# Optimization experiments

Hardware: AMD Instinct MI355X
Metric: run time of the kernel (lower is better)

The kernel has to match this reference:

```python
import jax, jax.numpy as jnp
import numpy as np

B, IN_DIM, Q_DIM, CODE_DIM, K, PROJ_DIM = 8192, 512, 128, 1024, 8, 64
NUM_LAYERS = 5
THRESHOLD = 0.9
SPARSITY_LEVELS = list(map(int, np.linspace(5, CODE_DIM, K)))  # matches torch default


def setup_inputs() -> dict:
    key = jax.random.key(0)
    ks = jax.random.split(key, 9)
    s = 0.02
    return {
        "x": jax.random.normal(ks[0], (B, IN_DIM), jnp.float32),
        "Wq": jax.random.normal(ks[1], (IN_DIM, Q_DIM), jnp.float32) * s,
        "bq": jnp.zeros((Q_DIM,), jnp.float32),
        "keys": jax.random.normal(ks[2], (K, Q_DIM), jnp.float32) * s,
        "We": jax.random.normal(ks[3], (K, IN_DIM, CODE_DIM), jnp.float32) * s,
        "S": jax.random.normal(ks[4], (K, CODE_DIM, CODE_DIM), jnp.float32) * s,
        "theta": jax.random.uniform(ks[5], (K,), jnp.float32) * 0.01,
        "W1": jax.random.normal(ks[6], (CODE_DIM, CODE_DIM), jnp.float32) * s,
        "b1": jnp.zeros((CODE_DIM,), jnp.float32),
        "W2": jax.random.normal(ks[7], (CODE_DIM, PROJ_DIM), jnp.float32) * s,
        "b2": jnp.zeros((PROJ_DIM,), jnp.float32),
    }


def _soft(z, theta):
    return jnp.sign(z) * jnp.maximum(jnp.abs(z) - theta, 0.0)


def reference(x, Wq, bq, keys, We, S, theta, W1, b1, W2, b2):
    # --- gating (attention): softmax(q @ keys^T / sqrt(d)) -> (B, K)
    q = x @ Wq + bq
    scores = (q @ keys.T) / jnp.sqrt(jnp.asarray(Q_DIM, x.dtype))
    gating_probs = jax.nn.softmax(scores, axis=-1)

    # --- all K LISTA experts densely: zs has shape (K, B, code_dim)
    Bx = jnp.einsum('bi,kic->kbc', x, We)            # (K, B, C)
    th = theta[:, None, None]
    z = _soft(Bx, th)
    for _ in range(NUM_LAYERS):
        z = _soft(Bx + jnp.einsum('kbc,kcd->kbd', z, S), th)

    # hard top-k (sparsity_level) magnitude pruning per expert
    pruned = []
    for k in range(K):
        zk = z[k]
        kk = SPARSITY_LEVELS[k]
        az = jnp.abs(zk)
        kth = jax.lax.top_k(az, kk)[0][:, -1]         # (B,)
        pruned.append(jnp.where(az >= kth[:, None], zk, 0.0))
    zs = jnp.stack(pruned, axis=0)                    # (K, B, C)

    # --- hard gating: among experts with p >= threshold*p_max, pick the
    # one with the smallest sparsity level (argmax always eligible, so the
    # empty-eligible branch in the torch code is unreachable for threshold<=1)
    p_max = jnp.max(gating_probs, axis=-1, keepdims=True)
    eligible = gating_probs >= THRESHOLD * p_max      # (B, K)
    sl = jnp.asarray(SPARSITY_LEVELS, jnp.float32)
    idx = jnp.argmin(jnp.where(eligible, sl[None, :], jnp.inf), axis=-1)  # (B,)

    selected_z = jnp.take_along_axis(zs, idx[None, :, None], axis=0)[0]   # (B, C)

    # --- projection head
    h = jax.nn.relu(selected_z @ W1 + b1)
    return h @ W2 + b2
```

## Files before the change

### kernel.cpp

```cpp
#include <hip/hip_runtime.h>
#include <math.h>

#define NB 8192
#define IND 512
#define QDIM 128
#define CD 1024
#define KE 8
#define PD 64
#define ORB 32

typedef _Float16 h8 __attribute__((ext_vector_type(8)));
typedef _Float16 h4 __attribute__((ext_vector_type(4)));
typedef float fx16 __attribute__((ext_vector_type(16)));

#define GLD16(g, l) __builtin_amdgcn_global_load_lds((const __attribute__((address_space(1))) void*)(g), (__attribute__((address_space(3))) void*)(l), 16, 0, 0)

__device__ __forceinline__ float softt(float v, float th) {
    float a = fabsf(v) - th;
    return a > 0.0f ? copysignf(a, v) : 0.0f;
}

__device__ __forceinline__ void fsplit(float v, _Float16& hi, _Float16& lo) {
    hi = (_Float16)v;
    lo = (_Float16)((v - (float)hi) * 2048.0f);
}

__global__ void k_precompute_M(const float* __restrict__ Wq, const float* __restrict__ keys,
                               const float* __restrict__ bq, float* __restrict__ M,
                               float* __restrict__ sb) {
    const float RSQ = 0.088388347648318447f;
    int g = blockIdx.x * 256 + threadIdx.x;
    if (g < IND * KE) {
        int i = g >> 3, k = g & 7;
        float s = 0.f;
        for (int q = 0; q < QDIM; ++q) s += Wq[i * QDIM + q] * keys[k * QDIM + q];
        M[g] = s * RSQ;
    }
    if (blockIdx.x == 0 && threadIdx.x < KE) {
        int k = threadIdx.x;
        float s = 0.f;
        for (int q = 0; q < QDIM; ++q) s += bq[q] * keys[k * QDIM + q];
        sb[k] = s * RSQ;
    }
}

__global__ __launch_bounds__(256)
void k_scores(const float* __restrict__ x, const float* __restrict__ M,
              const float* __restrict__ sb, int* __restrict__ idx) {
    __shared__ float Ms[KE][IND];
    __shared__ float sbs[KE];
    int t = threadIdx.x;
    #pragma unroll
    for (int j = 0; j < 16; ++j) {
        int e = j * 256 + t;
        Ms[e & 7][e >> 3] = M[e];
    }
    if (t < KE) sbs[t] = sb[t];
    __syncthreads();
    int w = t >> 6, lane = t & 63;
    int row = blockIdx.x * 4 + w;
    const float* xr = x + (size_t)row * IND;
    float sc[KE];
    #pragma unroll
    for (int k = 0; k < KE; ++k) sc[k] = 0.f;
    #pragma unroll
    for (int j = 0; j < IND / 64; ++j) {
        int ii = lane + 64 * j;
        float xv = xr[ii];
        #pragma unroll
        for (int k = 0; k < KE; ++k) sc[k] += xv * Ms[k][ii];
    }
    #pragma unroll
    for (int k = 0; k < KE; ++k) {
        #pragma unroll
        for (int off = 32; off >= 1; off >>= 1) sc[k] += __shfl_down(sc[k], off, 64);
    }
    if (lane == 0) {
        float smax = -1e30f;
        #pragma unroll
        for (int k = 0; k < KE; ++k) { sc[k] += sbs[k]; smax = fmaxf(smax, sc[k]); }
        const float LN09 = -0.105360515657826301f;
        int e = 0;
        #pragma unroll
        for (int k = KE - 1; k >= 0; --k)
            if (sc[k] >= smax + LN09) e = k;
        idx[row] = e;
    }
}

__global__ __launch_bounds__(256)
void k_count(const int* __restrict__ idx, int* __restrict__ perm,
             int* __restrict__ counts, int* __restrict__ offsets) {
    __shared__ int hist[256][KE];
    __shared__ int sc[2][KE][256];
    __shared__ int base[KE];
    const int t = threadIdx.x;
    int pc[KE];
    #pragma unroll
    for (int e = 0; e < KE; ++e) pc[e] = 0;
    for (int j = 0; j < NB / 256; ++j) pc[idx[j * 256 + t]]++;
    #pragma unroll
    for (int e = 0; e < KE; ++e) { hist[t][e] = pc[e]; sc[0][e][t] = pc[e]; }
    __syncthreads();
    int cur = 0;
    for (int d = 1; d < 256; d <<= 1) {
        #pragma unroll
        for (int e = 0; e < KE; ++e) {
            int v = sc[cur][e][t];
            if (t >= d) v += sc[cur][e][t - d];
            sc[cur ^ 1][e][t] = v;
        }
        cur ^= 1;
        __syncthreads();
    }
    if (t == 0) {
        int a = 0;
        #pragma unroll
        for (int e = 0; e < KE; ++e) {
            int tot = sc[cur][e][255];
            base[e] = a; offsets[e] = a; counts[e] = tot; a += tot;
        }
    }
    __syncthreads();
    int pos[KE];
    #pragma unroll
    for (int e = 0; e < KE; ++e) pos[e] = base[e] + sc[cur][e][t] - hist[t][e];
    for (int j = 0; j < NB / 256; ++j) {
        int r = j * 256 + t;
        int e = idx[r];
        perm[pos[e]++] = r;
    }
}

__global__ __launch_bounds__(256)
void k_split_rows(const float* __restrict__ src, _Float16* __restrict__ ph,
                  _Float16* __restrict__ pl, int n) {
    int i = (blockIdx.x * 256 + threadIdx.x) * 4;
    if (i < n) {
        float4 v = *(const float4*)(src + i);
        h4 hh, ll;
        #pragma unroll
        for (int j = 0; j < 4; ++j) {
            _Float16 a, b;
            fsplit((&v.x)[j], a, b);
            hh[j] = a; ll[j] = b;
        }
        *(h4*)(ph + i) = hh;
        *(h4*)(pl + i) = ll;
    }
}

__global__ __launch_bounds__(256)
void k_tsplit(const float* __restrict__ src, _Float16* __restrict__ th,
              _Float16* __restrict__ tl, int K, const int* __restrict__ counts) {
    int e = blockIdx.z;
    if (counts[e] == 0) return;
    __shared__ float tile[64][65];
    int k0 = blockIdx.x * 64;
    int n0 = blockIdx.y * 64;
    const float* s = src + (size_t)e * K * CD;
    int t = threadIdx.x;
    int tr = t >> 4;
    int tc = (t & 15) * 4;
    #pragma unroll
    for (int p = 0; p < 4; ++p) {
        int kk = tr + p * 16;
        float4 v = *(const float4*)&s[(size_t)(k0 + kk) * CD + n0 + tc];
        #pragma unroll
        for (int j = 0; j < 4; ++j) tile[kk][tc + j] = (&v.x)[j];
    }
    __syncthreads();
    int n = t >> 2;
    int kq = (t & 3) * 16;
    h8 hh0, hh1, ll0, ll1;
    #pragma unroll
    for (int j = 0; j < 8; ++j) {
        _Float16 a, b;
        fsplit(tile[kq + j][n], a, b);
        hh0[j] = a; ll0[j] = b;
        fsplit(tile[kq + 8 + j][n], a, b);
        hh1[j] = a; ll1[j] = b;
    }
    size_t ob = ((size_t)e * CD + n0 + n) * K + k0 + kq;
    *(h8*)(th + ob) = hh0;
    *(h8*)(th + ob + 8) = hh1;
    *(h8*)(tl + ob) = ll0;
    *(h8*)(tl + ob + 8) = ll1;
}

template <int KDIM, int MODE>
__global__ __launch_bounds__(256)
void k_mfma(const _Float16* __restrict__ Ah, const _Float16* __restrict__ Al,
            const _Float16* __restrict__ Bh, const _Float16* __restrict__ Bl,
            const float* __restrict__ theta, const float* __restrict__ BxBuf,
            float* __restrict__ BxOut, _Float16* __restrict__ zh, _Float16* __restrict__ zl,
            float* __restrict__ zf,
            const int* __restrict__ perm, const int* __restrict__ counts,
            const int* __restrict__ offsets) {
    const int e = blockIdx.z;
    const int cnt = counts[e];
    const int p = blockIdx.x + 8 * blockIdx.y;
    const int gx = p & 7;
    const int qq = p >> 3;
    const int bxl = qq & 7;
    const int byl = gx + 8 * (qq >> 3);
    const int m0 = byl * 128;
    if (m0 >= cnt) return;
    const int n0 = bxl * 128;
    const int off = offsets[e];
    const float th = theta[e];

    __shared__ _Float16 Asl[2][128 * 64];
    __shared__ _Float16 Bsl[2][128 * 64];

    const int t = threadIdx.x;
    const int lane = t & 63;
    const int w = t >> 6;

    const _Float16* aptr[4];
    const _Float16* bptr[4];
    #pragma unroll
    for (int i = 0; i < 4; ++i) {
        int s = w * 4 + i;
        int r = s * 8 + (lane >> 3);
        int pc = lane & 7;
        int lc = pc ^ ((r ^ (r >> 3)) & 7);
        int comp = lc & 1;
        int kg = lc >> 1;
        int mrow = m0 + r; if (mrow > cnt - 1) mrow = cnt - 1;
        size_t grow;
        if constexpr (MODE == 0) grow = (size_t)perm[off + mrow];
        else grow = (size_t)(off + mrow);
        aptr[i] = (comp ? Al : Ah) + grow * KDIM + kg * 8;
        bptr[i] = (comp ? Bl : Bh) + ((size_t)e * CD + n0 + r) * KDIM + kg * 8;
    }

    const int wm = w >> 1, wn = w & 1;
    const int q = lane >> 5;
    const int ml = lane & 31;

    fx16 acc1[2][2], acc2[2][2];
    #pragma unroll
    for (int mt = 0; mt < 2; ++mt)
        #pragma unroll
        for (int nt = 0; nt < 2; ++nt)
            #pragma unroll
            for (int g = 0; g < 16; ++g) { acc1[mt][nt][g] = 0.f; acc2[mt][nt][g] = 0.f; }

    auto stage = [&](int kt, int buf) {
        const int koff = kt * 32;
        #pragma unroll
        for (int i = 0; i < 4; ++i) {
            GLD16(aptr[i] + koff, &Asl[buf][(w * 4 + i) * 512]);
            GLD16(bptr[i] + koff, &Bsl[buf][(w * 4 + i) * 512]);
        }
    };

    const int NT = KDIM / 32;
    stage(0, 0);
    __syncthreads();
    for (int kt = 0; kt < NT; ++kt) {
        const int buf = kt & 1;
        if (kt + 1 < NT) stage(kt + 1, buf ^ 1);
        #pragma unroll
        for (int ks = 0; ks < 2; ++ks) {
            const int base = ks * 4 + q * 2;
            h8 ah[2], al2[2], bh2[2], bl2[2];
            #pragma unroll
            for (int mt = 0; mt < 2; ++mt) {
                int row = wm * 64 + mt * 32 + ml;
                int sw = (row ^ (row >> 3)) & 7;
                int mb = row * 64;
                ah[mt]  = *(const h8*)&Asl[buf][mb + (((base + 0) ^ sw) * 8)];
                al2[mt] = *(const h8*)&Asl[buf][mb + (((base + 1) ^ sw) * 8)];
            }
            #pragma unroll
            for (int nt = 0; nt < 2; ++nt) {
                int col = wn * 64 + nt * 32 + ml;
                int sw = (col ^ (col >> 3)) & 7;
                int nb = col * 64;
                bh2[nt] = *(const h8*)&Bsl[buf][nb + (((base + 0) ^ sw) * 8)];
                bl2[nt] = *(const h8*)&Bsl[buf][nb + (((base + 1) ^ sw) * 8)];
            }
            #pragma unroll
            for (int mt = 0; mt < 2; ++mt)
                #pragma unroll
                for (int nt = 0; nt < 2; ++nt) {
                    acc1[mt][nt] = __builtin_amdgcn_mfma_f32_32x32x16_f16(ah[mt],  bh2[nt], acc1[mt][nt], 0, 0, 0);
                    acc2[mt][nt] = __builtin_amdgcn_mfma_f32_32x32x16_f16(ah[mt],  bl2[nt], acc2[mt][nt], 0, 0, 0);
                    acc2[mt][nt] = __builtin_amdgcn_mfma_f32_32x32x16_f16(al2[mt], bh2[nt], acc2[mt][nt], 0, 0, 0);
                }
        }
        __syncthreads();
    }

    const float LSC = 4.8828125e-4f;
    #pragma unroll
    for (int mt = 0; mt < 2; ++mt)
        #pragma unroll
        for (int nt = 0; nt < 2; ++nt) {
            #pragma unroll
            for (int g = 0; g < 16; ++g) {
                int rl = wm * 64 + mt * 32 + (g & 3) + 8 * (g >> 2) + 4 * q;
                int mrow = m0 + rl;
                if (mrow < cnt) {
                    int col = n0 + wn * 64 + nt * 32 + ml;
                    size_t addr = (size_t)(off + mrow) * CD + col;
                    float v = acc1[mt][nt][g] + acc2[mt][nt][g] * LSC;
                    if constexpr (MODE == 0) {
                        BxOut[addr] = v;
                        float z = softt(v, th);
                        _Float16 a, b;
                        fsplit(z, a, b);
                        zh[addr] = a; zl[addr] = b;
                    } else if constexpr (MODE == 1) {
                        float z = softt(v + BxBuf[addr], th);
                        _Float16 a, b;
                        fsplit(z, a, b);
                        zh[addr] = a; zl[addr] = b;
                    } else {
                        zf[addr] = softt(v + BxBuf[addr], th);
                    }
                }
            }
        }
}

__global__ __launch_bounds__(256)
void k_prune(const float* __restrict__ z, const int* __restrict__ offsets,
             float* __restrict__ cval, int* __restrict__ cidx, int* __restrict__ rcnt) {
    const int SL[KE] = {5, 150, 296, 441, 587, 732, 878, 1024};
    const int t = threadIdx.x;
    const int lane = t & 63;
    const int wv = t >> 6;
    const int slot = blockIdx.x * 4 + wv;
    int k = 0;
    #pragma unroll
    for (int e = 1; e < KE; ++e)
        if (slot >= offsets[e]) k = e;
    const int lvl = SL[k];
    const float* zr = z + (size_t)slot * CD;
    float v[16];
    unsigned ab[16];
    #pragma unroll
    for (int j = 0; j < 16; ++j) {
        v[j] = zr[lane + 64 * j];
        ab[j] = __float_as_uint(fabsf(v[j]));
    }
    unsigned thr = 0;
    for (int b = 30; b >= 0; --b) {
        unsigned cand = thr | (1u << b);
        int c = 0;
        #pragma unroll
        for (int j = 0; j < 16; ++j) c += (ab[j] >= cand) ? 1 : 0;
        #pragma unroll
        for (int off = 1; off < 64; off <<= 1) c += __shfl_xor(c, off, 64);
        if (c >= lvl) thr = cand;
    }
    float* cvr = cval + (size_t)slot * CD;
    int* cir = cidx + (size_t)slot * CD;
    int base = 0;
    #pragma unroll
    for (int j = 0; j < 16; ++j) {
        bool keep = ab[j] >= thr;
        unsigned long long m = __ballot(keep);
        if (keep) {
            int pos = base + __popcll(m & ((1ULL << lane) - 1));
            cvr[pos] = v[j];
            cir[pos] = lane + 64 * j;
        }
        base += __popcll(m);
    }
    if (lane == 0) rcnt[slot] = base;
}

__global__ __launch_bounds__(256)
void k_output(const float* __restrict__ cval, const int* __restrict__ cidx,
              const int* __restrict__ rcnt,
              const float* __restrict__ W1, const float* __restrict__ b1,
              const float* __restrict__ W2, const float* __restrict__ b2,
              const int* __restrict__ perm, float* __restrict__ out) {
    __shared__ float W2s[64][68];
    __shared__ float hTs[64][34];
    __shared__ float cvS[ORB][16];
    __shared__ int   ciS[ORB][16];
    __shared__ int   cnS[ORB];

    const int t = threadIdx.x;
    const int s0 = blockIdx.x * ORB;

    if (t < ORB) cnS[t] = rcnt[s0 + t];
    __syncthreads();
    #pragma unroll
    for (int u = t; u < ORB * 16; u += 256) {
        int r = u >> 4, e = u & 15;
        int cnt = cnS[r];
        cvS[r][e] = (e < cnt) ? cval[(size_t)(s0 + r) * CD + e] : 0.f;
        ciS[r][e] = (e < cnt) ? cidx[(size_t)(s0 + r) * CD + e] : 0;
    }

    const int tm = t >> 4;
    const int tn = t & 15;
    const int iL = t & 63;
    const int rs = t >> 6;

    float acc0[4], acc1[4];
    #pragma unroll
    for (int j = 0; j < 4; ++j) { acc0[j] = 0.f; acc1[j] = 0.f; }

    for (int ch = 0; ch < 16; ++ch) {
        const int i0 = ch * 64;
        __syncthreads();
        #pragma unroll
        for (int p = 0; p < 4; ++p) {
            int kr = (t >> 4) + 16 * p;
            float4 w = *(const float4*)&W2[(size_t)(i0 + kr) * PD + (t & 15) * 4];
            *(float4*)&W2s[kr][(t & 15) * 4] = w;
        }
        float bv = b1[i0 + iL];
        #pragma unroll
        for (int jj = 0; jj < 8; ++jj) {
            int r = rs * 8 + jj;
            int cnt = cnS[r];
            float acc = bv;
            float wv[16];
            #pragma unroll
            for (int e = 0; e < 16; ++e)
                wv[e] = W1[(size_t)ciS[r][e] * CD + i0 + iL];
            #pragma unroll
            for (int e = 0; e < 16; ++e)
                acc = fmaf(cvS[r][e], wv[e], acc);
            if (cnt > 16) {
                const float* cvr = cval + (size_t)(s0 + r) * CD;
                const int* cir = cidx + (size_t)(s0 + r) * CD;
                for (int e = 16; e < cnt; ++e)
                    acc = fmaf(cvr[e], W1[(size_t)cir[e] * CD + i0 + iL], acc);
            }
            hTs[iL][r] = fmaxf(acc, 0.f);
        }
        __syncthreads();
        #pragma unroll 8
        for (int i = 0; i < 64; ++i) {
            float2 h2 = *(const float2*)&hTs[i][2 * tm];
            float4 w4 = *(const float4*)&W2s[i][4 * tn];
            const float* wp = &w4.x;
            #pragma unroll
            for (int j = 0; j < 4; ++j) {
                acc0[j] = fmaf(h2.x, wp[j], acc0[j]);
                acc1[j] = fmaf(h2.y, wp[j], acc1[j]);
            }
        }
    }

    float4 bb = *(const float4*)&b2[4 * tn];
    const float* bp = &bb.x;
    int g0 = perm[s0 + 2 * tm];
    int g1 = perm[s0 + 2 * tm + 1];
    float4 o0, o1;
    #pragma unroll
    for (int j = 0; j < 4; ++j) { (&o0.x)[j] = acc0[j] + bp[j]; (&o1.x)[j] = acc1[j] + bp[j]; }
    *(float4*)&out[(size_t)g0 * PD + 4 * tn] = o0;
    *(float4*)&out[(size_t)g1 * PD + 4 * tn] = o1;
}

extern "C" void kernel_launch(void* const* d_in, const int* in_sizes, int n_in,
                              void* d_out, int out_size, void* d_ws, size_t ws_size,
                              hipStream_t stream) {
    const float* x     = (const float*)d_in[0];
    const float* Wq    = (const float*)d_in[1];
    const float* bq    = (const float*)d_in[2];
    const float* keys  = (const float*)d_in[3];
    const float* We    = (const float*)d_in[4];
    const float* S     = (const float*)d_in[5];
    const float* theta = (const float*)d_in[6];
    const float* W1    = (const float*)d_in[7];
    const float* b1    = (const float*)d_in[8];
    const float* W2    = (const float*)d_in[9];
    const float* b2    = (const float*)d_in[10];
    float* out = (float*)d_out;

    const size_t F = (size_t)NB * CD;
    float* Bx = (float*)d_ws;
    _Float16* zAh = (_Float16*)(Bx + F);
    _Float16* zAl = zAh + F;
    float* R1 = (float*)(zAl + F);
    _Float16* xh  = (_Float16*)R1;
    _Float16* xl  = xh + (size_t)NB * IND;
    _Float16* weh = xl + (size_t)NB * IND;
    _Float16* wel = weh + (size_t)KE * IND * CD;
    _Float16* zBh = (_Float16*)R1;
    _Float16* zBl = zBh + F;
    float* z1 = R1;
    _Float16* sth = (_Float16*)(R1 + F);
    _Float16* stl = sth + F;
    float* M  = (float*)(stl + F);
    float* sb = M + IND * KE;
    int* idx     = (int*)(sb + 8);
    int* perm    = idx + NB;
    int* counts  = perm + NB;
    int* offsets = counts + KE;
    int* rcnt    = offsets + KE;
    float* cval = Bx;
    int*   cidx = (int*)zAh;

    k_precompute_M<<<16, 256, 0, stream>>>(Wq, keys, bq, M, sb);
    k_scores<<<NB / 4, 256, 0, stream>>>(x, M, sb, idx);
    k_count<<<1, 256, 0, stream>>>(idx, perm, counts, offsets);

    k_split_rows<<<(NB * IND) / 1024, 256, 0, stream>>>(x, xh, xl, NB * IND);
    {
        dim3 g(IND / 64, CD / 64, KE);
        k_tsplit<<<g, 256, 0, stream>>>(We, weh, wel, IND, counts);
    }
    {
        dim3 g(CD / 64, CD / 64, KE);
        k_tsplit<<<g, 256, 0, stream>>>(S, sth, stl, CD, counts);
    }

    dim3 gg(CD / 128, NB / 128, KE);
    k_mfma<IND, 0><<<gg, 256, 0, stream>>>(xh, xl, weh, wel, theta, nullptr, Bx, zAh, zAl, nullptr, perm, counts, offsets);
    k_mfma<CD, 1><<<gg, 256, 0, stream>>>(zAh, zAl, sth, stl, theta, Bx, nullptr, zBh, zBl, nullptr, perm, counts, offsets);
    k_mfma<CD, 1><<<gg, 256, 0, stream>>>(zBh, zBl, sth, stl, theta, Bx, nullptr, zAh, zAl, nullptr, perm, counts, offsets);
    k_mfma<CD, 1><<<gg, 256, 0, stream>>>(zAh, zAl, sth, stl, theta, Bx, nullptr, zBh, zBl, nullptr, perm, counts, offsets);
    k_mfma<CD, 1><<<gg, 256, 0, stream>>>(zBh, zBl, sth, stl, theta, Bx, nullptr, zAh, zAl, nullptr, perm, counts, offsets);
    k_mfma<CD, 2><<<gg, 256, 0, stream>>>(zAh, zAl, sth, stl, theta, Bx, nullptr, nullptr, nullptr, z1, perm, counts, offsets);

    k_prune<<<NB / 4, 256, 0, stream>>>(z1, offsets, cval, cidx, rcnt);
    k_output<<<NB / ORB, 256, 0, stream>>>(cval, cidx, rcnt, W1, b1, W2, b2, perm, out);
}
```

Measured before the change: 677.3 us.

## Fuse top-k pruning with sparse projection head into one per-row kernel

Merges the prune and output kernels into a single kernel in which each wavefront handles one row. It computes the magnitude threshold with ballot popcounts, compacts the kept entries into LDS, and accumulates the W1 rows for those entries straight into registers. It then applies ReLU and does the W2 projection in the same wavefront. This drops the compacted value/index round trip through global memory and one launch. In exchange, each row streams W1 rows with no cross-row reuse, and rows with more than 160 nonzeros fall back to a dense 1024-row loop, which could be costly for experts with high sparsity levels.

```diff
diff --git a/kernel.cpp b/kernel.cpp
--- a/kernel.cpp
+++ b/kernel.cpp
@@ -7,7 +7,7 @@
 #define CD 1024
 #define KE 8
 #define PD 64
-#define ORB 32
+#define PCAP 160
 
 typedef _Float16 h8 __attribute__((ext_vector_type(8)));
 typedef _Float16 h4 __attribute__((ext_vector_type(4)));
@@ -327,18 +327,28 @@
 }
 
 __global__ __launch_bounds__(256)
-void k_prune(const float* __restrict__ z, const int* __restrict__ offsets,
-             float* __restrict__ cval, int* __restrict__ cidx, int* __restrict__ rcnt) {
+void k_po(const float* __restrict__ z, const int* __restrict__ offsets,
+          const float* __restrict__ W1, const float* __restrict__ b1,
+          const float* __restrict__ W2, const float* __restrict__ b2,
+          const int* __restrict__ perm, float* __restrict__ out) {
     const int SL[KE] = {5, 150, 296, 441, 587, 732, 878, 1024};
+    __shared__ float vLg[4][PCAP];
+    __shared__ int   iLg[4][PCAP];
+    __shared__ float hSg[4][CD];
     const int t = threadIdx.x;
     const int lane = t & 63;
     const int wv = t >> 6;
     const int slot = blockIdx.x * 4 + wv;
+    float* vL = vLg[wv];
+    int* iLs = iLg[wv];
+    float* hS = hSg[wv];
+
     int k = 0;
     #pragma unroll
     for (int e = 1; e < KE; ++e)
         if (slot >= offsets[e]) k = e;
     const int lvl = SL[k];
+
     const float* zr = z + (size_t)slot * CD;
     float v[16];
     unsigned ab[16];
@@ -352,115 +362,75 @@
         unsigned cand = thr | (1u << b);
         int c = 0;
         #pragma unroll
-        for (int j = 0; j < 16; ++j) c += (ab[j] >= cand) ? 1 : 0;
-        #pragma unroll
-        for (int off = 1; off < 64; off <<= 1) c += __shfl_xor(c, off, 64);
+        for (int j = 0; j < 16; ++j)
+            c += __popcll(__ballot(ab[j] >= cand));
         if (c >= lvl) thr = cand;
     }
-    float* cvr = cval + (size_t)slot * CD;
-    int* cir = cidx + (size_t)slot * CD;
-    int base = 0;
-    #pragma unroll
-    for (int j = 0; j < 16; ++j) {
-        bool keep = ab[j] >= thr;
-        unsigned long long m = __ballot(keep);
-        if (keep) {
-            int pos = base + __popcll(m & ((1ULL << lane) - 1));
-            cvr[pos] = v[j];
-            cir[pos] = lane + 64 * j;
-        }
-        base += __popcll(m);
-    }
-    if (lane == 0) rcnt[slot] = base;
-}
-
-__global__ __launch_bounds__(256)
-void k_output(const float* __restrict__ cval, const int* __restrict__ cidx,
-              const int* __restrict__ rcnt,
-              const float* __restrict__ W1, const float* __restrict__ b1,
-              const float* __restrict__ W2, const float* __restrict__ b2,
-              const int* __restrict__ perm, float* __restrict__ out) {
-    __shared__ float W2s[64][68];
-    __shared__ float hTs[64][34];
-    __shared__ float cvS[ORB][16];
-    __shared__ int   ciS[ORB][16];
-    __shared__ int   cnS[ORB];
-
-    const int t = threadIdx.x;
-    const int s0 = blockIdx.x * ORB;
-
-    if (t < ORB) cnS[t] = rcnt[s0 + t];
-    __syncthreads();
-    #pragma unroll
-    for (int u = t; u < ORB * 16; u += 256) {
-        int r = u >> 4, e = u & 15;
-        int cnt = cnS[r];
-        cvS[r][e] = (e < cnt) ? cval[(size_t)(s0 + r) * CD + e] : 0.f;
-        ciS[r][e] = (e < cnt) ? cidx[(size_t)(s0 + r) * CD + e] : 0;
-    }
-
-    const int tm = t >> 4;
-    const int tn = t & 15;
-    const int iL = t & 63;
-    const int rs = t >> 6;
-
-    float acc0[4], acc1[4];
-    #pragma unroll
-    for (int j = 0; j < 4; ++j) { acc0[j] = 0.f; acc1[j] = 0.f; }
-
-    for (int ch = 0; ch < 16; ++ch) {
-        const int i0 = ch * 64;
-        __syncthreads();
-        #pragma unroll
-        for (int p = 0; p < 4; ++p) {
-            int kr = (t >> 4) + 16 * p;
-            float4 w = *(const float4*)&W2[(size_t)(i0 + kr) * PD + (t & 15) * 4];
-            *(float4*)&W2s[kr][(t & 15) * 4] = w;
-        }
-        float bv = b1[i0 + iL];
-        #pragma unroll
-        for (int jj = 0; jj < 8; ++jj) {
-            int r = rs * 8 + jj;
-            int cnt = cnS[r];
-            float acc = bv;
-            float wv[16];
-            #pragma unroll
-            for (int e = 0; e < 16; ++e)
-                wv[e] = W1[(size_t)ciS[r][e] * CD + i0 + iL];
-            #pragma unroll
-            for (int e = 0; e < 16; ++e)
-                acc = fmaf(cvS[r][e], wv[e], acc);
-            if (cnt > 16) {
-                const float* cvr = cval + (size_t)(s0 + r) * CD;
-                const int* cir = cidx + (size_t)(s0 + r) * CD;
-                for (int e = 16; e < cnt; ++e)
-                    acc = fmaf(cvr[e], W1[(size_t)cir[e] * CD + i0 + iL], acc);
+    int cnt = 0;
+    #pragma unroll
+    for (int j = 0; j < 16; ++j) cnt += __popcll(__ballot(ab[j] >= thr));
+
+    float h[16];
+    #pragma unroll
+    for (int j = 0; j < 16; ++j) h[j] = b1[lane + 64 * j];
+
+    if (cnt <= PCAP) {
+        int base = 0;
+        #pragma unroll
+        for (int j = 0; j < 16; ++j) {
+            bool keep = ab[j] >= thr;
+            unsigned long long m = __ballot(keep);
+            if (keep) {
+                int pos = base + __popcll(m & ((1ULL << lane) - 1));
+                vL[pos] = v[j];
+                iLs[pos] = lane + 64 * j;
             }
-            hTs[iL][r] = fmaxf(acc, 0.f);
-        }
-        __syncthreads();
-        #pragma unroll 8
-        for (int i = 0; i < 64; ++i) {
-            float2 h2 = *(const float2*)&hTs[i][2 * tm];
-            float4 w4 = *(const float4*)&W2s[i][4 * tn];
-            const float* wp = &w4.x;
-            #pragma unroll
-            for (int j = 0; j < 4; ++j) {
-                acc0[j] = fmaf(h2.x, wp[j], acc0[j]);
-                acc1[j] = fmaf(h2.y, wp[j], acc1[j]);
-            }
-        }
-    }
-
-    float4 bb = *(const float4*)&b2[4 * tn];
-    const float* bp = &bb.x;
-    int g0 = perm[s0 + 2 * tm];
-    int g1 = perm[s0 + 2 * tm + 1];
-    float4 o0, o1;
-    #pragma unroll
-    for (int j = 0; j < 4; ++j) { (&o0.x)[j] = acc0[j] + bp[j]; (&o1.x)[j] = acc1[j] + bp[j]; }
-    *(float4*)&out[(size_t)g0 * PD + 4 * tn] = o0;
-    *(float4*)&out[(size_t)g1 * PD + 4 * tn] = o1;
+            base += __popcll(m);
+        }
+        __builtin_amdgcn_wave_barrier();
+        for (int e = 0; e < cnt; ++e) {
+            float val = vL[e];
+            const float* wr = W1 + (size_t)iLs[e] * CD;
+            #pragma unroll
+            for (int j = 0; j < 16; ++j)
+                h[j] = fmaf(val, wr[lane + 64 * j], h[j]);
+        }
+    } else {
+        #pragma unroll
+        for (int j = 0; j < 16; ++j)
+            hS[lane + 64 * j] = (ab[j] >= thr) ? v[j] : 0.f;
+        __builtin_amdgcn_wave_barrier();
+        for (int e = 0; e < CD; ++e) {
+            float val = hS[e];
+            const float* wr = W1 + (size_t)e * CD;
+            #pragma unroll
+            for (int j = 0; j < 16; ++j)
+                h[j] = fmaf(val, wr[lane + 64 * j], h[j]);
+        }
+        __builtin_amdgcn_wave_barrier();
+    }
+
+    #pragma unroll
+    for (int j = 0; j < 16; ++j) hS[lane + 64 * j] = fmaxf(h[j], 0.f);
+    __builtin_amdgcn_wave_barrier();
+
+    const float* w2c = W2 + lane;
+    float a0 = 0.f, a1 = 0.f, a2 = 0.f, a3 = 0.f, a4 = 0.f, a5 = 0.f, a6 = 0.f, a7 = 0.f;
+    #pragma unroll 4
+    for (int i = 0; i < CD; i += 8) {
+        float4 h0 = *(const float4*)&hS[i];
+        float4 h1 = *(const float4*)&hS[i + 4];
+        a0 = fmaf(h0.x, w2c[(size_t)(i + 0) * PD], a0);
+        a1 = fmaf(h0.y, w2c[(size_t)(i + 1) * PD], a1);
+        a2 = fmaf(h0.z, w2c[(size_t)(i + 2) * PD], a2);
+        a3 = fmaf(h0.w, w2c[(size_t)(i + 3) * PD], a3);
+        a4 = fmaf(h1.x, w2c[(size_t)(i + 4) * PD], a4);
+        a5 = fmaf(h1.y, w2c[(size_t)(i + 5) * PD], a5);
+        a6 = fmaf(h1.z, w2c[(size_t)(i + 6) * PD], a6);
+        a7 = fmaf(h1.w, w2c[(size_t)(i + 7) * PD], a7);
+    }
+    float acc = ((a0 + a1) + (a2 + a3)) + ((a4 + a5) + (a6 + a7)) + b2[lane];
+    out[(size_t)perm[slot] * PD + lane] = acc;
 }
 
 extern "C" void kernel_launch(void* const* d_in, const int* in_sizes, int n_in,
@@ -499,9 +469,6 @@
     int* perm    = idx + NB;
     int* counts  = perm + NB;
     int* offsets = counts + KE;
-    int* rcnt    = offsets + KE;
-    float* cval = Bx;
-    int*   cidx = (int*)zAh;
 
     k_precompute_M<<<16, 256, 0, stream>>>(Wq, keys, bq, M, sb);
     k_scores<<<NB / 4, 256, 0, stream>>>(x, M, sb, idx);
@@ -525,6 +492,5 @@
     k_mfma<CD, 1><<<gg, 256, 0, stream>>>(zBh, zBl, sth, stl, theta, Bx, nullptr, zAh, zAl, nullptr, perm, counts, offsets);
     k_mfma<CD, 2><<<gg, 256, 0, stream>>>(zAh, zAl, sth, stl, theta, Bx, nullptr, nullptr, nullptr, z1, perm, counts, offsets);
 
-    k_prune<<<NB / 4, 256, 0, stream>>>(z1, offsets, cval, cidx, rcnt);
-    k_output<<<NB / ORB, 256, 0, stream>>>(cval, cidx, rcnt, W1, b1, W2, b2, perm, out);
-}
+    k_po<<<NB / 4, 256, 0, stream>>>(z1, offsets, W1, b1, W2, b2, perm, out);
+}
```

New measurement: 647.1 us. -4.5%, faster.
